# Kernel optimization log

Measured on AMD Instinct MI355X. Metric: run time of the kernel, lower is better.

## Reference

```python
import jax, jax.numpy as jnp
import numpy as np

DIM = 2048
N_HEADS = 32
N_KV_HEADS = 8
HEAD_DIM = 64
REPEATS = N_HEADS // N_KV_HEADS
SCALE = HEAD_DIM ** -0.5
L = 2048
B = 1


def rotary_matrix(context_len, d):
    # Dense (L, d, d) RoPE rotation matrix, exactly as get_rotary_matrix1.
    pos = jnp.arange(1, context_len + 1, dtype=jnp.float32)[:, None]
    i = jnp.arange(d // 2)
    theta = 10000.0 ** (-2.0 * i.astype(jnp.float32) / d)
    m_theta = pos * theta  # (L, d/2)
    cos_v, sin_v = jnp.cos(m_theta), jnp.sin(m_theta)
    R = jnp.zeros((context_len, d, d), dtype=jnp.float32)
    R = R.at[:, 2 * i, 2 * i].set(cos_v)
    R = R.at[:, 2 * i, 2 * i + 1].set(-sin_v)
    R = R.at[:, 2 * i + 1, 2 * i].set(sin_v)
    R = R.at[:, 2 * i + 1, 2 * i + 1].set(cos_v)
    return R


def causal_mask(context_len):
    idx = jnp.arange(context_len)
    return (idx[:, None] < idx[None, :]).astype(jnp.float32) * -1e9


def setup_inputs() -> dict:
    key = jax.random.key(0)
    ks = jax.random.split(key, 5)
    x = jax.random.normal(ks[0], (B, L, DIM), dtype=jnp.float32)
    mask = causal_mask(L)
    wq_w = jax.random.normal(ks[1], (N_HEADS * HEAD_DIM, DIM), dtype=jnp.float32) * 0.02
    wk_w = jax.random.normal(ks[2], (N_KV_HEADS * HEAD_DIM, DIM), dtype=jnp.float32) * 0.02
    wv_w = jax.random.normal(ks[3], (N_KV_HEADS * HEAD_DIM, DIM), dtype=jnp.float32) * 0.02
    wo_w = jax.random.normal(ks[4], (DIM, N_HEADS * HEAD_DIM), dtype=jnp.float32) * 0.02
    return {"x": x, "mask": mask, "wq_w": wq_w, "wk_w": wk_w, "wv_w": wv_w, "wo_w": wo_w}


def reference(x, mask, wq_w, wk_w, wv_w, wo_w):
    Bx, Lx, D = x.shape
    # projections (torch Linear: y = x @ W.T)
    q = jnp.einsum('bld,od->blo', x, wq_w).reshape(Bx, Lx, N_HEADS, HEAD_DIM).transpose(0, 2, 1, 3)
    k = jnp.einsum('bld,od->blo', x, wk_w).reshape(Bx, Lx, N_KV_HEADS, HEAD_DIM).transpose(0, 2, 1, 3)
    v = jnp.einsum('bld,od->blo', x, wv_w).reshape(Bx, Lx, N_KV_HEADS, HEAD_DIM).transpose(0, 2, 1, 3)
    # GQA repeat of kv heads (interleaved, matching concat-unsqueeze-reshape)
    k = jnp.repeat(k, REPEATS, axis=1)
    v = jnp.repeat(v, REPEATS, axis=1)
    # dense-matrix RoPE on q and (repeated) k
    R = rotary_matrix(Lx, HEAD_DIM)
    q = jnp.einsum('bhlj,lij->bhli', q, R)
    k = jnp.einsum('bhlj,lij->bhli', k, R)
    scores = jnp.einsum('bhld,bhmd->bhlm', q, k) * SCALE + mask
    attn = jax.nn.softmax(scores.astype(jnp.float32), axis=-1)
    out = jnp.einsum('bhlm,bhmd->bhld', attn, v)
    out = out.transpose(0, 2, 1, 3).reshape(Bx, Lx, N_HEADS * HEAD_DIM)
    out = jnp.einsum('blo,do->bld', out, wo_w)
    return out, k, v
```

## Files before the change

### kernel.cpp

```cpp
#include <hip/hip_runtime.h>

typedef __bf16 bf16;
typedef __bf16 bf16x8 __attribute__((ext_vector_type(8)));
typedef float floatx4 __attribute__((ext_vector_type(4)));
typedef float floatx16 __attribute__((ext_vector_type(16)));
typedef unsigned int uint;

#define MFMA16(a, b, c) __builtin_amdgcn_mfma_f32_16x16x32_bf16((a), (b), (c), 0, 0, 0)
#define MFMA32(a, b, c) __builtin_amdgcn_mfma_f32_32x32x16_bf16((a), (b), (c), 0, 0, 0)

__device__ __forceinline__ void gl2lds16(const bf16* g, bf16* l) {
  __builtin_amdgcn_global_load_lds(
      (const __attribute__((address_space(1))) void*)g,
      (__attribute__((address_space(3))) void*)l, 16, 0, 0);
}
__device__ __forceinline__ void wait_vm0() { __builtin_amdgcn_s_waitcnt(0x0f70); }

__device__ __forceinline__ void cvt8(const float* __restrict__ s,
                                     bf16* __restrict__ d, int i8) {
  const float4 a = ((const float4*)s)[i8 * 2];
  const float4 b = ((const float4*)s)[i8 * 2 + 1];
  bf16x8 o;
  o[0] = (bf16)a.x; o[1] = (bf16)a.y; o[2] = (bf16)a.z; o[3] = (bf16)a.w;
  o[4] = (bf16)b.x; o[5] = (bf16)b.y; o[6] = (bf16)b.z; o[7] = (bf16)b.w;
  *(bf16x8*)(d + i8 * 8) = o;
}

__global__ __launch_bounds__(256) void convert_kernel(
    const float* __restrict__ x, const float* __restrict__ wq,
    const float* __restrict__ wk, const float* __restrict__ wv,
    const float* __restrict__ wo, bf16* __restrict__ xb,
    bf16* __restrict__ wqb, bf16* __restrict__ wkb, bf16* __restrict__ wvb,
    bf16* __restrict__ wob) {
  const int g = blockIdx.x * 256 + threadIdx.x;
  if (g < 524288) cvt8(x, xb, g);
  else if (g < 1048576) cvt8(wq, wqb, g - 524288);
  else if (g < 1179648) cvt8(wk, wkb, g - 1048576);
  else if (g < 1310720) cvt8(wv, wvb, g - 1179648);
  else cvt8(wo, wob, g - 1310720);
}

template <typename OutT>
__device__ __forceinline__ void gemm_tile_body32(
    const bf16* __restrict__ A, int lda,
    const bf16* __restrict__ B, int ldb,
    OutT* __restrict__ C, int ldc, int K,
    bf16* As, bf16* Bs) {
  const int t = threadIdx.x;
  const int w = t >> 6, lane = t & 63;
  const int l15 = lane & 15, qd = lane >> 4;
  const int wr = w >> 1, wc = w & 1;

  floatx4 acc[4][4];
#pragma unroll
  for (int i = 0; i < 4; ++i)
#pragma unroll
    for (int j = 0; j < 4; ++j) acc[i][j] = (floatx4){0.f, 0.f, 0.f, 0.f};

  const int mt0 = w, mt1 = w + 4;
  const int kseg = qd * 8;
  const bf16* ga0 = A + (mt0 * 16 + l15) * lda + kseg;
  const bf16* ga1 = A + (mt1 * 16 + l15) * lda + kseg;
  const bf16* gb0 = B + (mt0 * 16 + l15) * ldb + kseg;
  const bf16* gb1 = B + (mt1 * 16 + l15) * ldb + kseg;
  bf16* lA0 = As + mt0 * 512 + lane * 8;
  bf16* lA1 = As + mt1 * 512 + lane * 8;
  bf16* lB0 = Bs + mt0 * 512 + lane * 8;
  bf16* lB1 = Bs + mt1 * 512 + lane * 8;

  for (int k0 = 0; k0 < K; k0 += 32) {
    gl2lds16(ga0 + k0, lA0);
    gl2lds16(ga1 + k0, lA1);
    gl2lds16(gb0 + k0, lB0);
    gl2lds16(gb1 + k0, lB1);
    wait_vm0();
    __syncthreads();

    bf16x8 a[4], b[4];
#pragma unroll
    for (int i = 0; i < 4; ++i)
      a[i] = *(const bf16x8*)(As + (wr * 4 + i) * 512 + lane * 8);
#pragma unroll
    for (int j = 0; j < 4; ++j)
      b[j] = *(const bf16x8*)(Bs + (wc * 4 + j) * 512 + lane * 8);
#pragma unroll
    for (int i = 0; i < 4; ++i)
#pragma unroll
      for (int j = 0; j < 4; ++j) acc[i][j] = MFMA16(a[i], b[j], acc[i][j]);
    __syncthreads();
  }

#pragma unroll
  for (int i = 0; i < 4; ++i)
#pragma unroll
    for (int j = 0; j < 4; ++j) {
      const int row = wr * 64 + i * 16 + qd * 4;
      const int col = wc * 64 + j * 16 + l15;
#pragma unroll
      for (int r = 0; r < 4; ++r)
        C[(row + r) * ldc + col] = (OutT)acc[i][j][r];
    }
}

template <typename OutT>
__device__ __forceinline__ void gemm_tile_body64(
    const bf16* __restrict__ A, int lda,
    const bf16* __restrict__ B, int ldb,
    OutT* __restrict__ C, int ldc, int K,
    bf16* S) {
  const int t = threadIdx.x;
  const int w = t >> 6, lane = t & 63;
  const int l15 = lane & 15, qd = lane >> 4;
  const int wr = w >> 1, wc = w & 1;

  floatx4 acc[2][4];
#pragma unroll
  for (int i = 0; i < 2; ++i)
#pragma unroll
    for (int j = 0; j < 4; ++j) acc[i][j] = (floatx4){0.f, 0.f, 0.f, 0.f};

  const bf16* gb[6];
  int lo[6];
#pragma unroll
  for (int i = 0; i < 6; ++i) {
    const int u = w + 4 * i;
    lo[i] = u * 512 + lane * 8;
    if (u < 8) {
      gb[i] = A + ((u >> 1) * 16 + l15) * lda + (u & 1) * 32 + qd * 8;
    } else {
      const int v = u - 8;
      gb[i] = B + ((v >> 1) * 16 + l15) * ldb + (v & 1) * 32 + qd * 8;
    }
  }

#define STG64(kt_, buf_)                                            \
  {                                                                 \
    bf16* d_ = S + (buf_) * 12288;                                  \
    _Pragma("unroll")                                               \
    for (int i_ = 0; i_ < 6; ++i_)                                  \
      gl2lds16(gb[i_] + (kt_) * 64, d_ + lo[i_]);                   \
  }

  const int NT = K >> 6;
  STG64(0, 0);
  wait_vm0();
  __syncthreads();
  int cur = 0;
  for (int kt = 0; kt < NT; ++kt) {
    if (kt + 1 < NT) STG64(kt + 1, cur ^ 1);
    const bf16* Ab = S + cur * 12288;
    const bf16* Bb = Ab + 4096;
    bf16x8 a[2][2], b[4][2];
#pragma unroll
    for (int i = 0; i < 2; ++i)
#pragma unroll
      for (int kk = 0; kk < 2; ++kk)
        a[i][kk] =
            *(const bf16x8*)(Ab + ((wr * 2 + i) * 2 + kk) * 512 + lane * 8);
#pragma unroll
    for (int j = 0; j < 4; ++j)
#pragma unroll
      for (int kk = 0; kk < 2; ++kk)
        b[j][kk] =
            *(const bf16x8*)(Bb + ((wc * 4 + j) * 2 + kk) * 512 + lane * 8);
#pragma unroll
    for (int kk = 0; kk < 2; ++kk)
#pragma unroll
      for (int i = 0; i < 2; ++i)
#pragma unroll
        for (int j = 0; j < 4; ++j)
          acc[i][j] = MFMA16(a[i][kk], b[j][kk], acc[i][j]);
    wait_vm0();
    __builtin_amdgcn_sched_barrier(0);
    __builtin_amdgcn_s_barrier();
    __builtin_amdgcn_sched_barrier(0);
    cur ^= 1;
  }
#undef STG64

#pragma unroll
  for (int i = 0; i < 2; ++i)
#pragma unroll
    for (int j = 0; j < 4; ++j) {
      const int row = wr * 32 + i * 16 + qd * 4;
      const int col = wc * 64 + j * 16 + l15;
#pragma unroll
      for (int r = 0; r < 4; ++r)
        C[(row + r) * ldc + col] = (OutT)acc[i][j][r];
    }
}

__global__ __launch_bounds__(256) void gemm_qkv(
    const bf16* __restrict__ x, const bf16* __restrict__ wq,
    const bf16* __restrict__ wk, const bf16* __restrict__ wv,
    bf16* __restrict__ Qws, bf16* __restrict__ Kws, bf16* __restrict__ Vws) {
  __shared__ bf16 As[4096], Bs[4096];
  const int bid = blockIdx.y * 24 + blockIdx.x;
  const int swz = (bid & 7) * 48 + (bid >> 3);
  const int nb = swz % 24;
  const int m0 = (swz / 24) * 128;
  const bf16* B;
  bf16* C;
  int ldc;
  if (nb < 16) {
    B = wq + nb * 128 * 2048;
    C = Qws + m0 * 2048 + nb * 128;
    ldc = 2048;
  } else if (nb < 20) {
    B = wk + (nb - 16) * 128 * 2048;
    C = Kws + m0 * 512 + (nb - 16) * 128;
    ldc = 512;
  } else {
    B = wv + (nb - 20) * 128 * 2048;
    C = Vws + m0 * 512 + (nb - 20) * 128;
    ldc = 512;
  }
  gemm_tile_body32<bf16>(x + m0 * 2048, 2048, B, 2048, C, ldc, 2048, As, Bs);
}

__global__ __launch_bounds__(256) void gemm_o(
    const bf16* __restrict__ Ows, const bf16* __restrict__ wo,
    float* __restrict__ out) {
  __shared__ bf16 S[24576];
  const int bid = blockIdx.y * 16 + blockIdx.x;
  const int swz = (bid & 7) * 64 + (bid >> 3);
  const int n0 = (swz & 15) * 128;
  const int m0 = (swz >> 4) * 64;
  gemm_tile_body64<float>(Ows + m0 * 2048, 2048, wo + n0 * 2048, 2048,
                          out + m0 * 2048 + n0, 2048, 2048, S);
}

__global__ __launch_bounds__(256) void rope_repeat_kernel(
    bf16* __restrict__ Qws, bf16* __restrict__ Kws, bf16* __restrict__ Kh,
    const bf16* __restrict__ Vws, bf16* __restrict__ Vt,
    float* __restrict__ kout, float* __restrict__ vout) {
  const int gid = blockIdx.x * 256 + threadIdx.x;
  const float NEG_LOG2_10000_D32 = -0.4152410118609203f;
  if (gid < 2097152) {
    const int l = gid >> 10, pr = gid & 1023, a = pr & 31;
    bf16* p = Qws + l * 2048 + pr * 2;
    const float x0 = (float)p[0], x1 = (float)p[1];
    const float ang = (float)(l + 1) * exp2f(NEG_LOG2_10000_D32 * (float)a);
    float s, c;
    __sincosf(ang, &s, &c);
    p[0] = (bf16)(c * x0 - s * x1);
    p[1] = (bf16)(s * x0 + c * x1);
  } else if (gid < 2097152 + 524288) {
    const int g = gid - 2097152;
    const int l = g >> 8, pr = g & 255, a = pr & 31, kvh = pr >> 5;
    bf16* p = Kws + l * 512 + pr * 2;
    const float x0 = (float)p[0], x1 = (float)p[1];
    const float ang = (float)(l + 1) * exp2f(NEG_LOG2_10000_D32 * (float)a);
    float s, c;
    __sincosf(ang, &s, &c);
    const float y0 = c * x0 - s * x1;
    const float y1 = s * x0 + c * x1;
    p[0] = (bf16)y0;
    p[1] = (bf16)y1;
    bf16* kp = Kh + (kvh * 2048 + l) * 64 + a * 2;
    kp[0] = (bf16)y0;
    kp[1] = (bf16)y1;
#pragma unroll
    for (int rep = 0; rep < 4; ++rep) {
      float* o = kout + (((kvh * 4 + rep) * 2048 + l) * 64 + a * 2);
      o[0] = y0;
      o[1] = y1;
    }
  } else if (gid < 2097152 + 524288 + 131072) {
    const int c = gid - (2097152 + 524288);
    const int l = c >> 6, seg = c & 63, kvh = seg >> 3;
    const bf16x8 v = *(const bf16x8*)(Vws + l * 512 + seg * 8);
    float4 f0, f1;
    f0.x = (float)v[0]; f0.y = (float)v[1]; f0.z = (float)v[2]; f0.w = (float)v[3];
    f1.x = (float)v[4]; f1.y = (float)v[5]; f1.z = (float)v[6]; f1.w = (float)v[7];
#pragma unroll
    for (int rep = 0; rep < 4; ++rep) {
      float* o = vout + (((kvh * 4 + rep) * 2048 + l) * 64 + (seg & 7) * 8);
      *(float4*)o = f0;
      *(float4*)(o + 4) = f1;
    }
  } else {
    const int c = gid - (2097152 + 524288 + 131072);
    const int kvh = c >> 14, r2 = c & 16383, dseg = r2 >> 11, l = r2 & 2047;
    const int d0 = dseg * 8;
    const bf16x8 v = *(const bf16x8*)(Vws + l * 512 + kvh * 64 + d0);
#pragma unroll
    for (int jj = 0; jj < 8; ++jj)
      Vt[kvh * 131072 + (d0 + jj) * 2048 + l] = v[jj];
  }
}

__global__ __launch_bounds__(256) void flash_kernel(
    const bf16* __restrict__ Qws, const bf16* __restrict__ Kh,
    const bf16* __restrict__ Vt, bf16* __restrict__ Ows,
    float* __restrict__ Opart, float* __restrict__ ML) {
  __shared__ bf16 KVs[2][2][4096];
  __shared__ bf16 Osh[128 * 66];

  const int h = blockIdx.y;
  const int bx = blockIdx.x;
  int qt, seg, kts, kte;
  if (bx < 8) {
    qt = bx; seg = -1; kts = 0; kte = 2 * qt + 2;
  } else {
    const int i = bx - 8;
    qt = 8 + (i >> 1);
    seg = i & 1;
    const int half = qt + 1;
    kts = seg * half;
    kte = kts + half;
  }
  const int kh = h >> 2;
  const int q0 = qt * 128;
  const int t = threadIdx.x, w = t >> 6, lane = t & 63;
  const int l31 = lane & 31, hf = lane >> 5;
  const int qw = q0 + w * 32;

  bf16x8 qf[4];
  {
    const bf16* qrow = Qws + (qw + l31) * 2048 + h * 64 + hf * 8;
#pragma unroll
    for (int c = 0; c < 4; ++c) qf[c] = *(const bf16x8*)(qrow + c * 16);
  }

  floatx16 o[2] = {};
  float mrun = -3e38f, lrun = 0.f;

  const int s0 = w, s1 = w + 4;
  const bf16* gK0 = Kh + kh * 131072 + ((s0 >> 2) * 32 + l31) * 64 + (s0 & 3) * 16 + hf * 8;
  const bf16* gK1 = Kh + kh * 131072 + ((s1 >> 2) * 32 + l31) * 64 + (s1 & 3) * 16 + hf * 8;
  const bf16* gV0 = Vt + kh * 131072 + ((s0 >> 2) * 32 + l31) * 2048 + (s0 & 3) * 16 + hf * 8;
  const bf16* gV1 = Vt + kh * 131072 + ((s1 >> 2) * 32 + l31) * 2048 + (s1 & 3) * 16 + hf * 8;

  {
    const int nb = kts & 1;
    gl2lds16(gK0 + kts * 4096, &KVs[nb][0][s0 * 512 + lane * 8]);
    gl2lds16(gK1 + kts * 4096, &KVs[nb][0][s1 * 512 + lane * 8]);
    gl2lds16(gV0 + kts * 64, &KVs[nb][1][s0 * 512 + lane * 8]);
    gl2lds16(gV1 + kts * 64, &KVs[nb][1][s1 * 512 + lane * 8]);
  }

  const float C = 0.1803368801f;
  for (int kt = kts; kt < kte; ++kt) {
    wait_vm0();
    __syncthreads();
    if (kt + 1 < kte) {
      const int nb = (kt + 1) & 1;
      const int koff = (kt + 1) * 4096, voff = (kt + 1) * 64;
      gl2lds16(gK0 + koff, &KVs[nb][0][s0 * 512 + lane * 8]);
      gl2lds16(gK1 + koff, &KVs[nb][0][s1 * 512 + lane * 8]);
      gl2lds16(gV0 + voff, &KVs[nb][1][s0 * 512 + lane * 8]);
      gl2lds16(gV1 + voff, &KVs[nb][1][s1 * 512 + lane * 8]);
    }
    const int kt64 = kt * 64;
    if (kt64 > qw + 31) continue;
    const bf16* Kb = &KVs[kt & 1][0][0];
    const bf16* Vb = &KVs[kt & 1][1][0];

    floatx16 st[2];
    __builtin_amdgcn_s_setprio(1);
#pragma unroll
    for (int tt = 0; tt < 2; ++tt) {
      floatx16 z = {};
#pragma unroll
      for (int c = 0; c < 4; ++c) {
        const bf16x8 kf = *(const bf16x8*)(Kb + (tt * 4 + c) * 512 + lane * 8);
        z = MFMA32(kf, qf[c], z);
      }
      st[tt] = z;
    }
    __builtin_amdgcn_s_setprio(0);
    if (kt64 + 64 > qw) {
      const int myq = qw + l31;
#pragma unroll
      for (int tt = 0; tt < 2; ++tt)
#pragma unroll
        for (int r = 0; r < 16; ++r) {
          const int key = kt64 + tt * 32 + (r & 3) + 8 * (r >> 2) + 4 * hf;
          if (key > myq) st[tt][r] = -1e30f;
        }
    }
    float ma = -3e38f, mb = -3e38f, mc = -3e38f, md = -3e38f;
#pragma unroll
    for (int tt = 0; tt < 2; ++tt)
#pragma unroll
      for (int r = 0; r < 16; r += 4) {
        ma = fmaxf(ma, st[tt][r + 0]);
        mb = fmaxf(mb, st[tt][r + 1]);
        mc = fmaxf(mc, st[tt][r + 2]);
        md = fmaxf(md, st[tt][r + 3]);
      }
    float mx = fmaxf(fmaxf(ma, mb), fmaxf(mc, md));
    mx = fmaxf(mx, __shfl_xor(mx, 32));
    const bool defer = __all((mx - mrun) * C <= 8.f);
    if (!defer) {
      const float mn = fmaxf(mrun, mx);
      const float al = __builtin_amdgcn_exp2f((mrun - mn) * C);
      lrun *= al;
#pragma unroll
      for (int n = 0; n < 2; ++n)
#pragma unroll
        for (int r = 0; r < 16; ++r) o[n][r] *= al;
      mrun = mn;
    }
    float ra = 0.f, rb = 0.f, rc = 0.f, rd = 0.f;
#pragma unroll
    for (int tt = 0; tt < 2; ++tt)
#pragma unroll
      for (int r = 0; r < 16; r += 4) {
        const float p0 = __builtin_amdgcn_exp2f((st[tt][r + 0] - mrun) * C);
        const float p1 = __builtin_amdgcn_exp2f((st[tt][r + 1] - mrun) * C);
        const float p2 = __builtin_amdgcn_exp2f((st[tt][r + 2] - mrun) * C);
        const float p3 = __builtin_amdgcn_exp2f((st[tt][r + 3] - mrun) * C);
        st[tt][r + 0] = p0; ra += p0;
        st[tt][r + 1] = p1; rb += p1;
        st[tt][r + 2] = p2; rc += p2;
        st[tt][r + 3] = p3; rd += p3;
      }
    float rs = (ra + rb) + (rc + rd);
    rs += __shfl_xor(rs, 32);
    lrun += rs;

    uint pk[2][4][2];
#pragma unroll
    for (int tt = 0; tt < 2; ++tt)
#pragma unroll
      for (int g = 0; g < 4; ++g)
#pragma unroll
        for (int p = 0; p < 2; ++p) {
          union { bf16 h2[2]; uint u; } cv;
          cv.h2[0] = (bf16)st[tt][4 * g + 2 * p];
          cv.h2[1] = (bf16)st[tt][4 * g + 2 * p + 1];
          pk[tt][g][p] = cv.u;
        }
    uint own_[2][2][2], rv[2][2][2];
#pragma unroll
    for (int tt = 0; tt < 2; ++tt)
#pragma unroll
      for (int gam = 0; gam < 2; ++gam)
#pragma unroll
        for (int p = 0; p < 2; ++p) {
          own_[tt][gam][p] = hf ? pk[tt][2 * gam + 1][p] : pk[tt][2 * gam][p];
          const uint snd = hf ? pk[tt][2 * gam][p] : pk[tt][2 * gam + 1][p];
          rv[tt][gam][p] = (uint)__shfl_xor((int)snd, 32);
        }
    __builtin_amdgcn_s_setprio(1);
#pragma unroll
    for (int c = 0; c < 4; ++c) {
      const int tt = c >> 1, gam = c & 1;
      union { uint u[4]; bf16x8 v; } pf;
      pf.u[0] = hf ? rv[tt][gam][0] : own_[tt][gam][0];
      pf.u[1] = hf ? rv[tt][gam][1] : own_[tt][gam][1];
      pf.u[2] = hf ? own_[tt][gam][0] : rv[tt][gam][0];
      pf.u[3] = hf ? own_[tt][gam][1] : rv[tt][gam][1];
#pragma unroll
      for (int n = 0; n < 2; ++n)
        o[n] = MFMA32(*(const bf16x8*)(Vb + (n * 4 + c) * 512 + lane * 8),
                      pf.v, o[n]);
    }
    __builtin_amdgcn_s_setprio(0);
  }

  if (seg < 0) {
    const float inv = 1.f / lrun;
#pragma unroll
    for (int n = 0; n < 2; ++n)
#pragma unroll
      for (int r = 0; r < 16; ++r) {
        const int dl = n * 32 + (r & 3) + 8 * (r >> 2) + 4 * hf;
        Osh[(w * 32 + l31) * 66 + dl] = (bf16)(o[n][r] * inv);
      }
    __syncthreads();
#pragma unroll
    for (int i = 0; i < 4; ++i) {
      const int row = (t >> 3) + i * 32;
      const int col = (t & 7) * 8;
      const bf16x8 vv = *(const bf16x8*)&Osh[row * 66 + col];
      *(bf16x8*)&Ows[(q0 + row) * 2048 + h * 64 + col] = vv;
    }
  } else {
    const int idx = (h * 8 + (qt - 8)) * 2 + seg;
    float* Op = Opart + idx * 8192;
#pragma unroll
    for (int n = 0; n < 2; ++n)
#pragma unroll
      for (int r = 0; r < 16; ++r) {
        const int dl = n * 32 + (r & 3) + 8 * (r >> 2) + 4 * hf;
        Op[dl * 128 + w * 32 + l31] = o[n][r];
      }
    if (hf == 0) {
      ML[idx * 256 + w * 32 + l31] = mrun;
      ML[idx * 256 + 128 + w * 32 + l31] = lrun;
    }
  }
}

__global__ __launch_bounds__(256) void combine_kernel(
    const float* __restrict__ Opart, const float* __restrict__ ML,
    bf16* __restrict__ Ows) {
  __shared__ bf16 Osh[128 * 66];
  const int b = blockIdx.x;
  const int h = b >> 3, qt = (b & 7) + 8;
  const int q0 = qt * 128;
  const int t = threadIdx.x;
  const int row = t & 127, dh = t >> 7;
  const int i0 = (h * 8 + (qt - 8)) * 2;
  const float C = 0.1803368801f;
  const float m0 = ML[i0 * 256 + row], l0 = ML[i0 * 256 + 128 + row];
  const float m1 = ML[(i0 + 1) * 256 + row], l1 = ML[(i0 + 1) * 256 + 128 + row];
  const float m = fmaxf(m0, m1);
  const float w0 = __builtin_amdgcn_exp2f((m0 - m) * C);
  const float w1 = __builtin_amdgcn_exp2f((m1 - m) * C);
  const float inv = 1.f / (l0 * w0 + l1 * w1);
  const float* P0 = Opart + i0 * 8192;
  const float* P1 = Opart + (i0 + 1) * 8192;
#pragma unroll
  for (int j = 0; j < 32; ++j) {
    const int d = dh * 32 + j;
    const float v = (P0[d * 128 + row] * w0 + P1[d * 128 + row] * w1) * inv;
    Osh[row * 66 + d] = (bf16)v;
  }
  __syncthreads();
#pragma unroll
  for (int i = 0; i < 4; ++i) {
    const int r2 = (t >> 3) + i * 32;
    const int col = (t & 7) * 8;
    const bf16x8 vv = *(const bf16x8*)&Osh[r2 * 66 + col];
    *(bf16x8*)&Ows[(q0 + r2) * 2048 + h * 64 + col] = vv;
  }
}

extern "C" void kernel_launch(void* const* d_in, const int* in_sizes, int n_in,
                              void* d_out, int out_size, void* d_ws,
                              size_t ws_size, hipStream_t stream) {
  const float* x = (const float*)d_in[0];
  const float* wq = (const float*)d_in[2];
  const float* wk = (const float*)d_in[3];
  const float* wv = (const float*)d_in[4];
  const float* wo = (const float*)d_in[5];

  float* out = (float*)d_out;
  float* kout = out + 4194304;
  float* vout = out + 8388608;

  bf16* ws = (bf16*)d_ws;
  bf16* xb = ws;
  bf16* wqb = xb + 4194304;
  bf16* wkb = wqb + 4194304;
  bf16* wvb = wkb + 1048576;
  bf16* wob = wvb + 1048576;
  bf16* Qws = wob + 4194304;
  bf16* Kws = Qws + 4194304;
  bf16* Vws = Kws + 1048576;
  bf16* Vt = Vws + 1048576;
  bf16* Ows = Vt + 1048576;
  bf16* Kh = Ows + 4194304;
  float* Opart = out;
  float* MLf = (float*)Kws;

  convert_kernel<<<dim3(7168), dim3(256), 0, stream>>>(x, wq, wk, wv, wo, xb,
                                                       wqb, wkb, wvb, wob);
  gemm_qkv<<<dim3(24, 16), dim3(256), 0, stream>>>(xb, wqb, wkb, wvb, Qws, Kws,
                                                   Vws);
  rope_repeat_kernel<<<dim3(11264), dim3(256), 0, stream>>>(Qws, Kws, Kh, Vws,
                                                            Vt, kout, vout);
  flash_kernel<<<dim3(24, 32), dim3(256), 0, stream>>>(Qws, Kh, Vt, Ows, Opart,
                                                       MLf);
  combine_kernel<<<dim3(256), dim3(256), 0, stream>>>(Opart, MLf, Ows);
  gemm_o<<<dim3(16, 32), dim3(256), 0, stream>>>(Ows, wob, out);
}
```

Baseline: 289.0 us.

## Fuse RoPE, GQA repeat and V transpose into QKV GEMM epilogue

Removes the separate rope_repeat kernel and applies RoPE, the K/V repeat outputs and the V transpose directly in the QKV GEMM epilogue. Pair partners are exchanged with a lane shuffle, since adjacent columns sit in adjacent lanes of the MFMA output. This saves a launch and a full read and write of the Q/K/V intermediates. In exchange the epilogue does uncoalesced scattered stores (strided Vt writes, per-element fp32 repeats) and extra sincos work per element inside the GEMM kernel.

```diff
diff --git a/kernel.cpp b/kernel.cpp
--- a/kernel.cpp
+++ b/kernel.cpp
@@ -41,68 +41,6 @@
 }
 
 template <typename OutT>
-__device__ __forceinline__ void gemm_tile_body32(
-    const bf16* __restrict__ A, int lda,
-    const bf16* __restrict__ B, int ldb,
-    OutT* __restrict__ C, int ldc, int K,
-    bf16* As, bf16* Bs) {
-  const int t = threadIdx.x;
-  const int w = t >> 6, lane = t & 63;
-  const int l15 = lane & 15, qd = lane >> 4;
-  const int wr = w >> 1, wc = w & 1;
-
-  floatx4 acc[4][4];
-#pragma unroll
-  for (int i = 0; i < 4; ++i)
-#pragma unroll
-    for (int j = 0; j < 4; ++j) acc[i][j] = (floatx4){0.f, 0.f, 0.f, 0.f};
-
-  const int mt0 = w, mt1 = w + 4;
-  const int kseg = qd * 8;
-  const bf16* ga0 = A + (mt0 * 16 + l15) * lda + kseg;
-  const bf16* ga1 = A + (mt1 * 16 + l15) * lda + kseg;
-  const bf16* gb0 = B + (mt0 * 16 + l15) * ldb + kseg;
-  const bf16* gb1 = B + (mt1 * 16 + l15) * ldb + kseg;
-  bf16* lA0 = As + mt0 * 512 + lane * 8;
-  bf16* lA1 = As + mt1 * 512 + lane * 8;
-  bf16* lB0 = Bs + mt0 * 512 + lane * 8;
-  bf16* lB1 = Bs + mt1 * 512 + lane * 8;
-
-  for (int k0 = 0; k0 < K; k0 += 32) {
-    gl2lds16(ga0 + k0, lA0);
-    gl2lds16(ga1 + k0, lA1);
-    gl2lds16(gb0 + k0, lB0);
-    gl2lds16(gb1 + k0, lB1);
-    wait_vm0();
-    __syncthreads();
-
-    bf16x8 a[4], b[4];
-#pragma unroll
-    for (int i = 0; i < 4; ++i)
-      a[i] = *(const bf16x8*)(As + (wr * 4 + i) * 512 + lane * 8);
-#pragma unroll
-    for (int j = 0; j < 4; ++j)
-      b[j] = *(const bf16x8*)(Bs + (wc * 4 + j) * 512 + lane * 8);
-#pragma unroll
-    for (int i = 0; i < 4; ++i)
-#pragma unroll
-      for (int j = 0; j < 4; ++j) acc[i][j] = MFMA16(a[i], b[j], acc[i][j]);
-    __syncthreads();
-  }
-
-#pragma unroll
-  for (int i = 0; i < 4; ++i)
-#pragma unroll
-    for (int j = 0; j < 4; ++j) {
-      const int row = wr * 64 + i * 16 + qd * 4;
-      const int col = wc * 64 + j * 16 + l15;
-#pragma unroll
-      for (int r = 0; r < 4; ++r)
-        C[(row + r) * ldc + col] = (OutT)acc[i][j][r];
-    }
-}
-
-template <typename OutT>
 __device__ __forceinline__ void gemm_tile_body64(
     const bf16* __restrict__ A, int lda,
     const bf16* __restrict__ B, int ldb,
@@ -193,29 +131,109 @@
 __global__ __launch_bounds__(256) void gemm_qkv(
     const bf16* __restrict__ x, const bf16* __restrict__ wq,
     const bf16* __restrict__ wk, const bf16* __restrict__ wv,
-    bf16* __restrict__ Qws, bf16* __restrict__ Kws, bf16* __restrict__ Vws) {
+    bf16* __restrict__ Qws, bf16* __restrict__ Kh, bf16* __restrict__ Vt,
+    float* __restrict__ kout, float* __restrict__ vout) {
   __shared__ bf16 As[4096], Bs[4096];
   const int bid = blockIdx.y * 24 + blockIdx.x;
   const int swz = (bid & 7) * 48 + (bid >> 3);
   const int nb = swz % 24;
   const int m0 = (swz / 24) * 128;
   const bf16* B;
-  bf16* C;
-  int ldc;
-  if (nb < 16) {
-    B = wq + nb * 128 * 2048;
-    C = Qws + m0 * 2048 + nb * 128;
-    ldc = 2048;
-  } else if (nb < 20) {
-    B = wk + (nb - 16) * 128 * 2048;
-    C = Kws + m0 * 512 + (nb - 16) * 128;
-    ldc = 512;
-  } else {
-    B = wv + (nb - 20) * 128 * 2048;
-    C = Vws + m0 * 512 + (nb - 20) * 128;
-    ldc = 512;
-  }
-  gemm_tile_body32<bf16>(x + m0 * 2048, 2048, B, 2048, C, ldc, 2048, As, Bs);
+  if (nb < 16) B = wq + nb * 128 * 2048;
+  else if (nb < 20) B = wk + (nb - 16) * 128 * 2048;
+  else B = wv + (nb - 20) * 128 * 2048;
+
+  const int t = threadIdx.x;
+  const int w = t >> 6, lane = t & 63;
+  const int l15 = lane & 15, qd = lane >> 4;
+  const int wr = w >> 1, wc = w & 1;
+
+  floatx4 acc[4][4];
+#pragma unroll
+  for (int i = 0; i < 4; ++i)
+#pragma unroll
+    for (int j = 0; j < 4; ++j) acc[i][j] = (floatx4){0.f, 0.f, 0.f, 0.f};
+
+  const bf16* A = x + m0 * 2048;
+  const int mt0 = w, mt1 = w + 4;
+  const int kseg = qd * 8;
+  const bf16* ga0 = A + (mt0 * 16 + l15) * 2048 + kseg;
+  const bf16* ga1 = A + (mt1 * 16 + l15) * 2048 + kseg;
+  const bf16* gb0 = B + (mt0 * 16 + l15) * 2048 + kseg;
+  const bf16* gb1 = B + (mt1 * 16 + l15) * 2048 + kseg;
+  bf16* lA0 = As + mt0 * 512 + lane * 8;
+  bf16* lA1 = As + mt1 * 512 + lane * 8;
+  bf16* lB0 = Bs + mt0 * 512 + lane * 8;
+  bf16* lB1 = Bs + mt1 * 512 + lane * 8;
+
+  for (int k0 = 0; k0 < 2048; k0 += 32) {
+    gl2lds16(ga0 + k0, lA0);
+    gl2lds16(ga1 + k0, lA1);
+    gl2lds16(gb0 + k0, lB0);
+    gl2lds16(gb1 + k0, lB1);
+    wait_vm0();
+    __syncthreads();
+
+    bf16x8 a[4], b[4];
+#pragma unroll
+    for (int i = 0; i < 4; ++i)
+      a[i] = *(const bf16x8*)(As + (wr * 4 + i) * 512 + lane * 8);
+#pragma unroll
+    for (int j = 0; j < 4; ++j)
+      b[j] = *(const bf16x8*)(Bs + (wc * 4 + j) * 512 + lane * 8);
+#pragma unroll
+    for (int i = 0; i < 4; ++i)
+#pragma unroll
+      for (int j = 0; j < 4; ++j) acc[i][j] = MFMA16(a[i], b[j], acc[i][j]);
+    __syncthreads();
+  }
+
+  const float NEG_LOG2_10000_D32 = -0.4152410118609203f;
+  const int odd = l15 & 1;
+#pragma unroll
+  for (int i = 0; i < 4; ++i)
+#pragma unroll
+    for (int j = 0; j < 4; ++j) {
+      const int row = wr * 64 + i * 16 + qd * 4;
+      const int col = wc * 64 + j * 16 + l15;
+#pragma unroll
+      for (int r = 0; r < 4; ++r) {
+        const float own = acc[i][j][r];
+        const int rg = m0 + row + r;
+        if (nb < 16) {
+          const float part = __shfl_xor(own, 1);
+          const int gcol = nb * 128 + col;
+          const int a = (gcol & 63) >> 1;
+          const float ang =
+              (float)(rg + 1) * exp2f(NEG_LOG2_10000_D32 * (float)a);
+          float s, c;
+          __sincosf(ang, &s, &c);
+          const float val = odd ? (s * part + c * own) : (c * own - s * part);
+          Qws[rg * 2048 + gcol] = (bf16)val;
+        } else if (nb < 20) {
+          const float part = __shfl_xor(own, 1);
+          const int g512 = (nb - 16) * 128 + col;
+          const int kvh = g512 >> 6, d = g512 & 63;
+          const int a = d >> 1;
+          const float ang =
+              (float)(rg + 1) * exp2f(NEG_LOG2_10000_D32 * (float)a);
+          float s, c;
+          __sincosf(ang, &s, &c);
+          const float val = odd ? (s * part + c * own) : (c * own - s * part);
+          Kh[(kvh * 2048 + rg) * 64 + d] = (bf16)val;
+          float* o = kout + (kvh * 4 * 2048 + rg) * 64 + d;
+#pragma unroll
+          for (int rep = 0; rep < 4; ++rep) o[rep * 131072] = val;
+        } else {
+          const int g512 = (nb - 20) * 128 + col;
+          const int kvh = g512 >> 6, d = g512 & 63;
+          float* o = vout + (kvh * 4 * 2048 + rg) * 64 + d;
+#pragma unroll
+          for (int rep = 0; rep < 4; ++rep) o[rep * 131072] = own;
+          Vt[kvh * 131072 + d * 2048 + rg] = (bf16)own;
+        }
+      }
+    }
 }
 
 __global__ __launch_bounds__(256) void gemm_o(
@@ -228,66 +246,6 @@
   const int m0 = (swz >> 4) * 64;
   gemm_tile_body64<float>(Ows + m0 * 2048, 2048, wo + n0 * 2048, 2048,
                           out + m0 * 2048 + n0, 2048, 2048, S);
-}
-
-__global__ __launch_bounds__(256) void rope_repeat_kernel(
-    bf16* __restrict__ Qws, bf16* __restrict__ Kws, bf16* __restrict__ Kh,
-    const bf16* __restrict__ Vws, bf16* __restrict__ Vt,
-    float* __restrict__ kout, float* __restrict__ vout) {
-  const int gid = blockIdx.x * 256 + threadIdx.x;
-  const float NEG_LOG2_10000_D32 = -0.4152410118609203f;
-  if (gid < 2097152) {
-    const int l = gid >> 10, pr = gid & 1023, a = pr & 31;
-    bf16* p = Qws + l * 2048 + pr * 2;
-    const float x0 = (float)p[0], x1 = (float)p[1];
-    const float ang = (float)(l + 1) * exp2f(NEG_LOG2_10000_D32 * (float)a);
-    float s, c;
-    __sincosf(ang, &s, &c);
-    p[0] = (bf16)(c * x0 - s * x1);
-    p[1] = (bf16)(s * x0 + c * x1);
-  } else if (gid < 2097152 + 524288) {
-    const int g = gid - 2097152;
-    const int l = g >> 8, pr = g & 255, a = pr & 31, kvh = pr >> 5;
-    bf16* p = Kws + l * 512 + pr * 2;
-    const float x0 = (float)p[0], x1 = (float)p[1];
-    const float ang = (float)(l + 1) * exp2f(NEG_LOG2_10000_D32 * (float)a);
-    float s, c;
-    __sincosf(ang, &s, &c);
-    const float y0 = c * x0 - s * x1;
-    const float y1 = s * x0 + c * x1;
-    p[0] = (bf16)y0;
-    p[1] = (bf16)y1;
-    bf16* kp = Kh + (kvh * 2048 + l) * 64 + a * 2;
-    kp[0] = (bf16)y0;
-    kp[1] = (bf16)y1;
-#pragma unroll
-    for (int rep = 0; rep < 4; ++rep) {
-      float* o = kout + (((kvh * 4 + rep) * 2048 + l) * 64 + a * 2);
-      o[0] = y0;
-      o[1] = y1;
-    }
-  } else if (gid < 2097152 + 524288 + 131072) {
-    const int c = gid - (2097152 + 524288);
-    const int l = c >> 6, seg = c & 63, kvh = seg >> 3;
-    const bf16x8 v = *(const bf16x8*)(Vws + l * 512 + seg * 8);
-    float4 f0, f1;
-    f0.x = (float)v[0]; f0.y = (float)v[1]; f0.z = (float)v[2]; f0.w = (float)v[3];
-    f1.x = (float)v[4]; f1.y = (float)v[5]; f1.z = (float)v[6]; f1.w = (float)v[7];
-#pragma unroll
-    for (int rep = 0; rep < 4; ++rep) {
-      float* o = vout + (((kvh * 4 + rep) * 2048 + l) * 64 + (seg & 7) * 8);
-      *(float4*)o = f0;
-      *(float4*)(o + 4) = f1;
-    }
-  } else {
-    const int c = gid - (2097152 + 524288 + 131072);
-    const int kvh = c >> 14, r2 = c & 16383, dseg = r2 >> 11, l = r2 & 2047;
-    const int d0 = dseg * 8;
-    const bf16x8 v = *(const bf16x8*)(Vws + l * 512 + kvh * 64 + d0);
-#pragma unroll
-    for (int jj = 0; jj < 8; ++jj)
-      Vt[kvh * 131072 + (d0 + jj) * 2048 + l] = v[jj];
-  }
 }
 
 __global__ __launch_bounds__(256) void flash_kernel(
@@ -560,10 +518,8 @@
 
   convert_kernel<<<dim3(7168), dim3(256), 0, stream>>>(x, wq, wk, wv, wo, xb,
                                                        wqb, wkb, wvb, wob);
-  gemm_qkv<<<dim3(24, 16), dim3(256), 0, stream>>>(xb, wqb, wkb, wvb, Qws, Kws,
-                                                   Vws);
-  rope_repeat_kernel<<<dim3(11264), dim3(256), 0, stream>>>(Qws, Kws, Kh, Vws,
-                                                            Vt, kout, vout);
+  gemm_qkv<<<dim3(24, 16), dim3(256), 0, stream>>>(xb, wqb, wkb, wvb, Qws, Kh,
+                                                   Vt, kout, vout);
   flash_kernel<<<dim3(24, 32), dim3(256), 0, stream>>>(Qws, Kh, Vt, Ows, Opart,
                                                        MLf);
   combine_kernel<<<dim3(256), dim3(256), 0, stream>>>(Opart, MLf, Ows);
```

Measured after the change: 288.7 us. About the same (-0.1%).
